# Kernel optimization log

Measured on AMD Instinct MI355X. Metric: run time of the kernel, lower is better.

## Reference

```python
import jax, jax.numpy as jnp
import numpy as np
import math

DIM = 2880
N_HEADS = 64
N_KV = 8
HEAD_DIM = 64
WINDOW = 128          # layer_id = 0 (even) -> sliding window active
BASE = 150000.0
INIT_CTX = 4096
SCALE = 32.0
NTK_ALPHA = 1.0
NTK_BETA = 32.0
EPS = 1e-5
SEQ = 1536
BATCH = 1
SM_SCALE = 1.0 / math.sqrt(HEAD_DIM)


def _rope_tables(seq_len):
    """YaRN (NTK-by-parts) cos/sin tables, half-split convention. [S, D/2]."""
    freq = BASE ** (np.arange(0, HEAD_DIM, 2, dtype=np.float32) / HEAD_DIM)
    concentration = 0.1 * math.log(SCALE) + 1.0
    d_half = HEAD_DIM / 2
    low = d_half * math.log(INIT_CTX / (NTK_BETA * 2 * math.pi)) / math.log(BASE)
    high = d_half * math.log(INIT_CTX / (NTK_ALPHA * 2 * math.pi)) / math.log(BASE)
    interpolation = 1.0 / (SCALE * freq)
    extrapolation = 1.0 / freq
    ramp = (np.arange(d_half, dtype=np.float32) - low) / (high - low)
    mask = 1.0 - np.clip(ramp, 0.0, 1.0)
    inv_freq = interpolation * (1.0 - mask) + extrapolation * mask
    t = np.arange(seq_len, dtype=np.float32)
    freqs = np.outer(t, inv_freq)
    return (jnp.asarray(np.cos(freqs) * concentration),
            jnp.asarray(np.sin(freqs) * concentration))


def _apply_rope(x, cos, sin):
    # x: [B, S, H, D]; cos/sin: [S, D/2]
    c = cos[None, :, None, :]
    s = sin[None, :, None, :]
    x1, x2 = jnp.split(x, 2, axis=-1)
    return jnp.concatenate([x1 * c - x2 * s, x2 * c + x1 * s], axis=-1)


def setup_inputs() -> dict:
    key = jax.random.key(0)
    ks = jax.random.split(key, 5)
    x = jax.random.normal(ks[0], (BATCH, SEQ, DIM), dtype=jnp.float32)
    sinks = jax.random.normal(ks[1], (N_HEADS,), dtype=jnp.float32)
    norm_w = jnp.ones((DIM,), dtype=jnp.float32)
    qkv_dim = HEAD_DIM * (N_HEADS + 2 * N_KV)  # 5120
    qkv_w = jax.random.normal(ks[2], (qkv_dim, DIM), dtype=jnp.float32) / math.sqrt(DIM)
    qkv_b = jnp.zeros((qkv_dim,), dtype=jnp.float32)
    out_w = jax.random.normal(ks[3], (DIM, N_HEADS * HEAD_DIM), dtype=jnp.float32) / math.sqrt(N_HEADS * HEAD_DIM)
    out_b = jnp.zeros((DIM,), dtype=jnp.float32)
    return {"x": x, "sinks": sinks, "norm_w": norm_w, "qkv_w": qkv_w,
            "qkv_b": qkv_b, "out_w": out_w, "out_b": out_b}


def reference(x, sinks, norm_w, qkv_w, qkv_b, out_w, out_b):
    B, S, _ = x.shape
    # RMSNorm
    t = x * jax.lax.rsqrt(jnp.mean(x * x, axis=-1, keepdims=True) + EPS) * norm_w
    # fused QKV projection
    qkv = t @ qkv_w.T + qkv_b
    q_dim = N_HEADS * HEAD_DIM
    kv_dim = N_KV * HEAD_DIM
    q = qkv[..., :q_dim].reshape(B, S, N_HEADS, HEAD_DIM)
    k = qkv[..., q_dim:q_dim + kv_dim].reshape(B, S, N_KV, HEAD_DIM)
    v = qkv[..., q_dim + kv_dim:].reshape(B, S, N_KV, HEAD_DIM)
    # YaRN RoPE
    cos, sin = _rope_tables(S)
    q = _apply_rope(q, cos, sin)
    k = _apply_rope(k, cos, sin)
    # GQA: group query heads per kv head
    G = N_HEADS // N_KV
    qg = q.reshape(B, S, N_KV, G, HEAD_DIM)
    scores = jnp.einsum('bqkgd,bskd->bkgqs', qg, k) * SM_SCALE  # [B,KV,G,Sq,Sk]
    # causal + sliding-window mask
    i = jnp.arange(S)[:, None]
    j = jnp.arange(S)[None, :]
    allowed = j <= i
    if WINDOW > 0:
        allowed = allowed & ((i - j) < WINDOW)
    scores = jnp.where(allowed, scores, -jnp.inf)
    # sink tokens: one extra learned logit per head in the softmax denominator
    sink = sinks.reshape(N_KV, G)[None, :, :, None, None]
    sink = jnp.broadcast_to(sink, (B, N_KV, G, S, 1))
    logits = jnp.concatenate([scores, sink], axis=-1)  # [B,KV,G,Sq,Sk+1]
    p = jax.nn.softmax(logits, axis=-1)[..., :S]        # drop sink column
    attn = jnp.einsum('bkgqs,bskd->bqkgd', p, v).reshape(B, S, N_HEADS * HEAD_DIM)
    return attn @ out_w.T + out_b
```

## Files before the change

### kernel.cpp

```cpp
#include <hip/hip_runtime.h>

typedef unsigned short u16;
typedef unsigned int u32;
typedef __bf16 bf16x8 __attribute__((ext_vector_type(8)));
typedef float f32x4 __attribute__((ext_vector_type(4)));

#define S_LEN 1536
#define DIM 2880
#define NQH 64
#define NKVH 8
#define HD 64
#define QKV_N 5120
#define QDIM 4096
#define KVDIM 512
#define WIN 128
#define SM_SCALE 0.125f

__device__ __forceinline__ u16 f2bf(float f) {
  union { float f; u32 u; } a; a.f = f;
  u32 u = a.u;
  u32 lsb = (u >> 16) & 1;
  u += 0x7fffu + lsb;
  return (u16)(u >> 16);
}
__device__ __forceinline__ u32 pk2bf(float a, float b) {
  return (u32)f2bf(a) | ((u32)f2bf(b) << 16);
}

#define GLOAD16(g, l) __builtin_amdgcn_global_load_lds( \
    (const __attribute__((address_space(1))) u32*)(g), \
    (__attribute__((address_space(3))) u32*)(l), 16, 0, 0)

__global__ void rope_tables(float* __restrict__ cosT, float* __restrict__ sinT) {
  int idx = blockIdx.x * blockDim.x + threadIdx.x;
  if (idx >= S_LEN * 32) return;
  int s = idx >> 5, d = idx & 31;
  const double TWO_PI = 6.283185307179586;
  double freq = pow(150000.0, (double)d / 32.0);
  double conc = 0.1 * log(32.0) + 1.0;
  double lb = log(150000.0);
  double low = 32.0 * log(4096.0 / (32.0 * TWO_PI)) / lb;
  double high = 32.0 * log(4096.0 / (1.0 * TWO_PI)) / lb;
  double interp = 1.0 / (32.0 * freq), extra = 1.0 / freq;
  double ramp = ((double)d - low) / (high - low);
  ramp = ramp < 0.0 ? 0.0 : (ramp > 1.0 ? 1.0 : ramp);
  double maskv = 1.0 - ramp;
  double invf = interp * (1.0 - maskv) + extra * maskv;
  double ang = (double)s * invf;
  cosT[idx] = (float)(cos(ang) * conc);
  sinT[idx] = (float)(sin(ang) * conc);
}

__global__ __launch_bounds__(256) void rmsnorm_bf16(
    const float* __restrict__ x, const float* __restrict__ wgt,
    u16* __restrict__ th) {
  int row = blockIdx.x;
  const float* xr = x + (size_t)row * DIM;
  float ss = 0.f;
  for (int i = threadIdx.x; i < DIM / 4; i += 256) {
    float4 v = *(const float4*)&xr[i * 4];
    ss += v.x * v.x + v.y * v.y + v.z * v.z + v.w * v.w;
  }
  for (int m = 32; m >= 1; m >>= 1) ss += __shfl_xor(ss, m);
  __shared__ float red[4];
  int lane = threadIdx.x & 63, w = threadIdx.x >> 6;
  if (lane == 0) red[w] = ss;
  __syncthreads();
  float tot = red[0] + red[1] + red[2] + red[3];
  float scale = rsqrtf(tot / (float)DIM + 1e-5f);
  for (int i = threadIdx.x; i < DIM / 4; i += 256) {
    float4 v = *(const float4*)&xr[i * 4];
    float4 g = *(const float4*)&wgt[i * 4];
    ushort4 hi;
    hi.x = f2bf(v.x * scale * g.x);
    hi.y = f2bf(v.y * scale * g.y);
    hi.z = f2bf(v.z * scale * g.z);
    hi.w = f2bf(v.w * scale * g.w);
    *(ushort4*)&th[(size_t)row * DIM + i * 4] = hi;
  }
}

__global__ __launch_bounds__(256) void conv2(
    const float* __restrict__ s1, u16* __restrict__ d1, long n1,
    const float* __restrict__ s2, u16* __restrict__ d2, long n2) {
  long idx = (long)blockIdx.x * 256 + threadIdx.x;
  const float* src; u16* dst; long i;
  if (idx < n1) { src = s1; dst = d1; i = idx; }
  else if (idx < n1 + n2) { src = s2; dst = d2; i = idx - n1; }
  else return;
  float4 v = *(const float4*)&src[i * 4];
  ushort4 h;
  h.x = f2bf(v.x); h.y = f2bf(v.y); h.z = f2bf(v.z); h.w = f2bf(v.w);
  *(ushort4*)&dst[i * 4] = h;
}


__global__ __launch_bounds__(256, 4) void gemm_rope(
    const u16* __restrict__ A, const u16* __restrict__ B,
    const float* __restrict__ bias,
    const float* __restrict__ cosT, const float* __restrict__ sinT,
    u16* __restrict__ Qb, u16* __restrict__ Kb, u16* __restrict__ Vt) {
  __shared__ u16 As[3 * 2048];
  __shared__ u16 Bs[3 * 4096];
  const int K = DIM;
  const int t = threadIdx.x;
  const int lane = t & 63, w = t >> 6;

  const int nby = gridDim.y;
  const int nwg = gridDim.x * nby;
  int orig = blockIdx.x * nby + blockIdx.y;
  {
    int q = nwg >> 3, r = nwg & 7;
    int xcd = orig & 7, i = orig >> 3;
    orig = (xcd < r ? xcd * (q + 1) : r * (q + 1) + (xcd - r) * q) + i;
  }
  const int m0 = (orig % nby) * 64, n0 = (orig / nby) * 128;

  const int wr = (w >> 1) * 32, wc = (w & 1) * 64;
  const int lr = lane & 15, lk8 = (lane >> 4) * 8;
  const int lcol = lk8 ^ (((lr >> 1) & 3) << 3);
  const int g4 = (lane >> 4) * 4;
  f32x4 acc[2][4] = {};

  const size_t ga  = (size_t)(m0 + (t >> 2)) * K + (((t & 3) ^ ((t >> 3) & 3)) * 8);
  const size_t gb0 = (size_t)(n0 + (t >> 2)) * K + (((t & 3) ^ ((t >> 3) & 3)) * 8);
  const size_t gb1 = (size_t)(n0 + 64 + (t >> 2)) * K + (((t & 3) ^ ((t >> 3) & 3)) * 8);

  auto STAGE = [&](int buf, int k0) {
    GLOAD16(A + ga + k0,  &As[buf * 2048 + t * 8]);
    GLOAD16(B + gb0 + k0, &Bs[buf * 4096 + t * 8]);
    GLOAD16(B + gb1 + k0, &Bs[buf * 4096 + (t + 256) * 8]);
  };

  const int nk = K / 32;
  STAGE(0, 0); STAGE(1, 32);

  for (int tt = 0; tt < nk; ++tt) {
    const int cur = tt % 3;
    if (tt + 1 < nk) {
      asm volatile("s_waitcnt vmcnt(6)" ::: "memory");
    } else {
      asm volatile("s_waitcnt vmcnt(0)" ::: "memory");
    }
    __builtin_amdgcn_s_barrier();
    __builtin_amdgcn_sched_barrier(0);
    if (tt + 2 < nk) STAGE((tt + 2) % 3, (tt + 2) * 32);
    const u16* as_ = &As[cur * 2048];
    const u16* bs_ = &Bs[cur * 4096];
    bf16x8 af[2], bf_[4];
#pragma unroll
    for (int i = 0; i < 2; ++i) af[i] = *(const bf16x8*)&as_[(wr + i * 16 + lr) * 32 + lcol];
#pragma unroll
    for (int j = 0; j < 4; ++j) bf_[j] = *(const bf16x8*)&bs_[(wc + j * 16 + lr) * 32 + lcol];
    __builtin_amdgcn_s_setprio(1);
#pragma unroll
    for (int i = 0; i < 2; ++i)
#pragma unroll
      for (int j = 0; j < 4; ++j)
        acc[i][j] = __builtin_amdgcn_mfma_f32_16x16x32_bf16(af[i], bf_[j], acc[i][j], 0, 0, 0);
    __builtin_amdgcn_s_setprio(0);
  }

  if (n0 < 4608) {
    const bool isQ = (n0 < 4096);
    const float sc = isQ ? SM_SCALE : 1.0f;
#pragma unroll
    for (int i = 0; i < 2; ++i) {
      const int row = m0 + wr + i * 16 + g4;
#pragma unroll
      for (int j = 0; j < 2; ++j) {
        const int col = n0 + wc + j * 16 + lr;
        const int d = j * 16 + lr;
        const float b1 = bias[col], b2 = bias[col + 32];
#pragma unroll
        for (int r = 0; r < 4; ++r) {
          const float c = cosT[(row + r) * 32 + d];
          const float s = sinT[(row + r) * 32 + d];
          const float x1 = acc[i][j][r] + b1;
          const float x2 = acc[i][j + 2][r] + b2;
          const float o1 = (x1 * c - x2 * s) * sc;
          const float o2 = (x2 * c + x1 * s) * sc;
          if (isQ) {
            Qb[(size_t)(row + r) * QDIM + col] = f2bf(o1);
            Qb[(size_t)(row + r) * QDIM + col + 32] = f2bf(o2);
          } else {
            Kb[(size_t)(row + r) * KVDIM + (col - 4096)] = f2bf(o1);
            Kb[(size_t)(row + r) * KVDIM + (col - 4096) + 32] = f2bf(o2);
          }
        }
      }
    }
  } else {
#pragma unroll
    for (int i = 0; i < 2; ++i) {
      const int rowb = m0 + wr + i * 16 + g4;
#pragma unroll
      for (int j = 0; j < 4; ++j) {
        const int col = n0 + wc + j * 16 + lr;
        const float bb = bias[col];
        ushort4 pk;
        pk.x = f2bf(acc[i][j][0] + bb);
        pk.y = f2bf(acc[i][j][1] + bb);
        pk.z = f2bf(acc[i][j][2] + bb);
        pk.w = f2bf(acc[i][j][3] + bb);
        *(ushort4*)&Vt[(size_t)(col - 4608) * S_LEN + rowb] = pk;
      }
    }
  }
}

__global__ __launch_bounds__(256, 4) void gemm_bt(
    const u16* __restrict__ A, const u16* __restrict__ B,
    const float* __restrict__ bias, float* __restrict__ C,
    int M, int N, int K) {
  __shared__ u16 As[3 * 2048];
  __shared__ u16 Bs[3 * 4096];
  const int t = threadIdx.x;
  const int lane = t & 63, w = t >> 6;

  const int nby = gridDim.y;
  const int nwg = gridDim.x * nby;
  int orig = blockIdx.x * nby + blockIdx.y;
  {
    int q = nwg >> 3, r = nwg & 7;
    int xcd = orig & 7, i = orig >> 3;
    orig = (xcd < r ? xcd * (q + 1) : r * (q + 1) + (xcd - r) * q) + i;
  }
  const int m0 = (orig % nby) * 64, n0 = (orig / nby) * 128;

  const int wr = (w >> 1) * 32, wc = (w & 1) * 64;
  const int lr = lane & 15, lk8 = (lane >> 4) * 8;
  const int lcol = lk8 ^ (((lr >> 1) & 3) << 3);
  const int g4 = (lane >> 4) * 4;
  f32x4 acc[2][4] = {};

  int rB0 = n0 + (t >> 2); if (rB0 > N - 1) rB0 = N - 1;
  int rB1 = n0 + 64 + (t >> 2); if (rB1 > N - 1) rB1 = N - 1;
  const size_t ga  = (size_t)(m0 + (t >> 2)) * K + (((t & 3) ^ ((t >> 3) & 3)) * 8);
  const size_t gb0 = (size_t)rB0 * K + (((t & 3) ^ ((t >> 3) & 3)) * 8);
  const size_t gb1 = (size_t)rB1 * K + (((t & 3) ^ ((t >> 3) & 3)) * 8);

  auto STAGE = [&](int buf, int k0) {
    GLOAD16(A + ga + k0,  &As[buf * 2048 + t * 8]);
    GLOAD16(B + gb0 + k0, &Bs[buf * 4096 + t * 8]);
    GLOAD16(B + gb1 + k0, &Bs[buf * 4096 + (t + 256) * 8]);
  };

  const int nk = K / 32;
  STAGE(0, 0); STAGE(1, 32);

  for (int tt = 0; tt < nk; ++tt) {
    const int cur = tt % 3;
    if (tt + 1 < nk) {
      asm volatile("s_waitcnt vmcnt(6)" ::: "memory");
    } else {
      asm volatile("s_waitcnt vmcnt(0)" ::: "memory");
    }
    __builtin_amdgcn_s_barrier();
    __builtin_amdgcn_sched_barrier(0);
    if (tt + 2 < nk) STAGE((tt + 2) % 3, (tt + 2) * 32);
    const u16* as_ = &As[cur * 2048];
    const u16* bs_ = &Bs[cur * 4096];
    bf16x8 af[2], bf_[4];
#pragma unroll
    for (int i = 0; i < 2; ++i) af[i] = *(const bf16x8*)&as_[(wr + i * 16 + lr) * 32 + lcol];
#pragma unroll
    for (int j = 0; j < 4; ++j) bf_[j] = *(const bf16x8*)&bs_[(wc + j * 16 + lr) * 32 + lcol];
    __builtin_amdgcn_s_setprio(1);
#pragma unroll
    for (int i = 0; i < 2; ++i)
#pragma unroll
      for (int j = 0; j < 4; ++j)
        acc[i][j] = __builtin_amdgcn_mfma_f32_16x16x32_bf16(af[i], bf_[j], acc[i][j], 0, 0, 0);
    __builtin_amdgcn_s_setprio(0);
  }

#pragma unroll
  for (int i = 0; i < 2; ++i) {
    const int row = m0 + wr + i * 16 + g4;
#pragma unroll
    for (int j = 0; j < 4; ++j) {
      const int col = n0 + wc + j * 16 + lr;
      if (col < N) {
        const float bb = bias[col];
#pragma unroll
        for (int r = 0; r < 4; ++r)
          C[(size_t)(row + r) * N + col] = acc[i][j][r] + bb;
      }
    }
  }
}

__global__ __launch_bounds__(256) void attn2(
    const u16* __restrict__ Q, const u16* __restrict__ Kb, const u16* __restrict__ Vt,
    const float* __restrict__ sinks, u16* __restrict__ O) {
  const int h = blockIdx.x;
  const int kh = h >> 3;
  const int wid = threadIdx.x >> 6;
  const int lane = threadIdx.x & 63;
  const int q0 = blockIdx.y * 128 + wid * 32;
  const int lr = lane & 15;
  const int g = lane >> 4;

  bf16x8 bq[2][2];
#pragma unroll
  for (int qf = 0; qf < 2; ++qf)
#pragma unroll
    for (int kc = 0; kc < 2; ++kc)
      bq[qf][kc] = *(const bf16x8*)&Q[(size_t)(q0 + qf * 16 + lr) * QDIM + h * HD + kc * 32 + g * 8];

  f32x4 o[2][4] = {};
  float m_s[2] = {-1e30f, -1e30f};
  float l_s[2] = {0.f, 0.f};

  int js = q0 - 128; if (js < 0) js = 0;

  for (int j0 = js; j0 <= q0; j0 += 32) {
    bf16x8 ak[2][2];
#pragma unroll
    for (int jf = 0; jf < 2; ++jf)
#pragma unroll
      for (int kc = 0; kc < 2; ++kc)
        ak[jf][kc] = *(const bf16x8*)&Kb[(size_t)(j0 + jf * 16 + lr) * KVDIM + kh * HD + kc * 32 + g * 8];

    f32x4 st[2][2] = {};
#pragma unroll
    for (int jf = 0; jf < 2; ++jf)
#pragma unroll
      for (int qf = 0; qf < 2; ++qf) {
        st[jf][qf] = __builtin_amdgcn_mfma_f32_16x16x32_bf16(ak[jf][0], bq[qf][0], st[jf][qf], 0, 0, 0);
        st[jf][qf] = __builtin_amdgcn_mfma_f32_16x16x32_bf16(ak[jf][1], bq[qf][1], st[jf][qf], 0, 0, 0);
      }

    float pv[2][2][4];
    float tmax[2] = {-1e30f, -1e30f};
#pragma unroll
    for (int jf = 0; jf < 2; ++jf)
#pragma unroll
      for (int qf = 0; qf < 2; ++qf)
#pragma unroll
        for (int r = 0; r < 4; ++r) {
          int jv = j0 + jf * 16 + 4 * g + r;
          int qq = q0 + qf * 16 + lr;
          float sc = st[jf][qf][r];
          bool ok = (jv <= qq) && (qq - jv < WIN);
          sc = ok ? sc : -1e30f;
          pv[jf][qf][r] = sc;
          tmax[qf] = fmaxf(tmax[qf], sc);
        }
#pragma unroll
    for (int qf = 0; qf < 2; ++qf) {
      float tm = tmax[qf];
      tm = fmaxf(tm, __shfl_xor(tm, 16));
      tm = fmaxf(tm, __shfl_xor(tm, 32));
      const float mo = m_s[qf];
      const float mn = fmaxf(mo, tm);
      const float esc = __expf(mo - mn);
      float ps = 0.f;
#pragma unroll
      for (int jf = 0; jf < 2; ++jf)
#pragma unroll
        for (int r = 0; r < 4; ++r) {
          float sv = pv[jf][qf][r];
          float e = __expf(sv - mn);
          e = (sv <= -1e29f) ? 0.f : e;
          pv[jf][qf][r] = e;
          ps += e;
        }
      ps += __shfl_xor(ps, 16);
      ps += __shfl_xor(ps, 32);
      l_s[qf] = l_s[qf] * esc + ps;
      m_s[qf] = mn;
#pragma unroll
      for (int df = 0; df < 4; ++df) o[qf][df] *= esc;
    }

    bf16x8 pb[2];
    const int srcA = lr + ((g & 1) ? 32 : 0);
    const int srcB = srcA + 16;
    const bool hi_half = (g >= 2);
#pragma unroll
    for (int qf = 0; qf < 2; ++qf) {
      u32 w0a = pk2bf(pv[0][qf][0], pv[0][qf][1]);
      u32 w1a = pk2bf(pv[0][qf][2], pv[0][qf][3]);
      u32 w0b = pk2bf(pv[1][qf][0], pv[1][qf][1]);
      u32 w1b = pk2bf(pv[1][qf][2], pv[1][qf][3]);
      u32 a0 = (u32)__shfl((int)w0a, srcA, 64);
      u32 a1 = (u32)__shfl((int)w1a, srcA, 64);
      u32 a2 = (u32)__shfl((int)w0a, srcB, 64);
      u32 a3 = (u32)__shfl((int)w1a, srcB, 64);
      u32 b0 = (u32)__shfl((int)w0b, srcA, 64);
      u32 b1 = (u32)__shfl((int)w1b, srcA, 64);
      u32 b2 = (u32)__shfl((int)w0b, srcB, 64);
      u32 b3 = (u32)__shfl((int)w1b, srcB, 64);
      union { u32 d[4]; bf16x8 v; } u_;
      u_.d[0] = hi_half ? b0 : a0;
      u_.d[1] = hi_half ? b1 : a1;
      u_.d[2] = hi_half ? b2 : a2;
      u_.d[3] = hi_half ? b3 : a3;
      pb[qf] = u_.v;
    }

    bf16x8 av[4];
#pragma unroll
    for (int df = 0; df < 4; ++df)
      av[df] = *(const bf16x8*)&Vt[((size_t)kh * HD + df * 16 + lr) * S_LEN + j0 + g * 8];

#pragma unroll
    for (int qf = 0; qf < 2; ++qf)
#pragma unroll
      for (int df = 0; df < 4; ++df)
        o[qf][df] = __builtin_amdgcn_mfma_f32_16x16x32_bf16(av[df], pb[qf], o[qf][df], 0, 0, 0);
  }

  const float snk = sinks[h];
#pragma unroll
  for (int qf = 0; qf < 2; ++qf) {
    const float mo = m_s[qf];
    const float Mx = fmaxf(mo, snk);
    const float den = l_s[qf] * __expf(mo - Mx) + __expf(snk - Mx);
    const float osc = __expf(mo - Mx) / den;
    const int row = q0 + qf * 16 + lr;
#pragma unroll
    for (int df = 0; df < 4; ++df) {
      ushort4 pk;
      pk.x = f2bf(o[qf][df][0] * osc);
      pk.y = f2bf(o[qf][df][1] * osc);
      pk.z = f2bf(o[qf][df][2] * osc);
      pk.w = f2bf(o[qf][df][3] * osc);
      *(ushort4*)&O[(size_t)row * QDIM + h * HD + df * 16 + 4 * g] = pk;
    }
  }
}

extern "C" void kernel_launch(void* const* d_in, const int* in_sizes, int n_in,
                              void* d_out, int out_size, void* d_ws, size_t ws_size,
                              hipStream_t stream) {
  const float* x      = (const float*)d_in[0];
  const float* sinks  = (const float*)d_in[1];
  const float* norm_w = (const float*)d_in[2];
  const float* qkv_w  = (const float*)d_in[3];
  const float* qkv_b  = (const float*)d_in[4];
  const float* out_w  = (const float*)d_in[5];
  const float* out_b  = (const float*)d_in[6];
  float* out = (float*)d_out;

  char* ws = (char*)d_ws;
  size_t off = 0;
  auto take = [&](size_t bytes) -> void* {
    void* r = ws + off;
    off += (bytes + 255) & ~(size_t)255;
    return r;
  };
  float* cosT = (float*)take((size_t)S_LEN * 32 * 4);
  float* sinT = (float*)take((size_t)S_LEN * 32 * 4);
  u16* th  = (u16*)take((size_t)S_LEN * DIM * 2);
  u16* wh  = (u16*)take((size_t)QKV_N * DIM * 2);
  u16* ow  = (u16*)take((size_t)DIM * QDIM * 2);
  u16* Qb  = (u16*)take((size_t)S_LEN * QDIM * 2);
  u16* Kb  = (u16*)take((size_t)S_LEN * KVDIM * 2);
  u16* Vt  = (u16*)take((size_t)S_LEN * KVDIM * 2);
  u16* Ab  = (u16*)take((size_t)S_LEN * QDIM * 2);

  const long n1 = (long)QKV_N * DIM / 4;
  const long n2 = (long)DIM * QDIM / 4;

  rope_tables<<<(S_LEN * 32 + 255) / 256, 256, 0, stream>>>(cosT, sinT);
  rmsnorm_bf16<<<S_LEN, 256, 0, stream>>>(x, norm_w, th);
  conv2<<<(int)((n1 + n2 + 255) / 256), 256, 0, stream>>>(qkv_w, wh, n1, out_w, ow, n2);
  gemm_rope<<<dim3(QKV_N / 128, S_LEN / 64), 256, 0, stream>>>(
      th, wh, qkv_b, cosT, sinT, Qb, Kb, Vt);
  attn2<<<dim3(NQH, S_LEN / 128), 256, 0, stream>>>(Qb, Kb, Vt, sinks, Ab);
  gemm_bt<<<dim3((DIM + 127) / 128, S_LEN / 64), 256, 0, stream>>>(
      Ab, ow, out_b, out, S_LEN, DIM, QDIM);
}
```

Before: 216.6 us.

## Enlarge GEMM tiles to 128x128 and issue prefetch before the wait

Both bf16 GEMMs (QKV+RoPE and output projection) now compute 128x128 output tiles per block, with each wave holding a 64x64 accumulator, instead of 64x128. This halves the A/B tile reloads from global memory and raises MFMA work per LDS read. The next-stage global load is now issued before the vmcnt wait, with an extra end-of-iteration barrier protecting buffer reuse. The trade-offs are higher register and LDS use (occupancy hint lowered to 3) and a grid of fewer blocks, which may leave CUs idle or poorly balanced.

```diff
diff --git a/kernel.cpp b/kernel.cpp
--- a/kernel.cpp
+++ b/kernel.cpp
@@ -95,12 +95,12 @@
 }
 
 
-__global__ __launch_bounds__(256, 4) void gemm_rope(
+__global__ __launch_bounds__(256, 3) void gemm_rope(
     const u16* __restrict__ A, const u16* __restrict__ B,
     const float* __restrict__ bias,
     const float* __restrict__ cosT, const float* __restrict__ sinT,
     u16* __restrict__ Qb, u16* __restrict__ Kb, u16* __restrict__ Vt) {
-  __shared__ u16 As[3 * 2048];
+  __shared__ u16 As[3 * 4096];
   __shared__ u16 Bs[3 * 4096];
   const int K = DIM;
   const int t = threadIdx.x;
@@ -114,20 +114,23 @@
     int xcd = orig & 7, i = orig >> 3;
     orig = (xcd < r ? xcd * (q + 1) : r * (q + 1) + (xcd - r) * q) + i;
   }
-  const int m0 = (orig % nby) * 64, n0 = (orig / nby) * 128;
-
-  const int wr = (w >> 1) * 32, wc = (w & 1) * 64;
+  const int m0 = (orig % nby) * 128, n0 = (orig / nby) * 128;
+
+  const int wr = (w >> 1) * 64, wc = (w & 1) * 64;
   const int lr = lane & 15, lk8 = (lane >> 4) * 8;
   const int lcol = lk8 ^ (((lr >> 1) & 3) << 3);
   const int g4 = (lane >> 4) * 4;
-  f32x4 acc[2][4] = {};
-
-  const size_t ga  = (size_t)(m0 + (t >> 2)) * K + (((t & 3) ^ ((t >> 3) & 3)) * 8);
-  const size_t gb0 = (size_t)(n0 + (t >> 2)) * K + (((t & 3) ^ ((t >> 3) & 3)) * 8);
-  const size_t gb1 = (size_t)(n0 + 64 + (t >> 2)) * K + (((t & 3) ^ ((t >> 3) & 3)) * 8);
+  f32x4 acc[4][4] = {};
+
+  const int ks = ((t & 3) ^ ((t >> 3) & 3)) * 8;
+  const size_t ga0 = (size_t)(m0 + (t >> 2)) * K + ks;
+  const size_t ga1 = (size_t)(m0 + 64 + (t >> 2)) * K + ks;
+  const size_t gb0 = (size_t)(n0 + (t >> 2)) * K + ks;
+  const size_t gb1 = (size_t)(n0 + 64 + (t >> 2)) * K + ks;
 
   auto STAGE = [&](int buf, int k0) {
-    GLOAD16(A + ga + k0,  &As[buf * 2048 + t * 8]);
+    GLOAD16(A + ga0 + k0, &As[buf * 4096 + t * 8]);
+    GLOAD16(A + ga1 + k0, &As[buf * 4096 + (t + 256) * 8]);
     GLOAD16(B + gb0 + k0, &Bs[buf * 4096 + t * 8]);
     GLOAD16(B + gb1 + k0, &Bs[buf * 4096 + (t + 256) * 8]);
   };
@@ -137,35 +140,39 @@
 
   for (int tt = 0; tt < nk; ++tt) {
     const int cur = tt % 3;
-    if (tt + 1 < nk) {
-      asm volatile("s_waitcnt vmcnt(6)" ::: "memory");
+    if (tt + 2 < nk) {
+      STAGE((tt + 2) % 3, (tt + 2) * 32);
+      asm volatile("s_waitcnt vmcnt(8)" ::: "memory");
+    } else if (tt + 1 < nk) {
+      asm volatile("s_waitcnt vmcnt(4)" ::: "memory");
     } else {
       asm volatile("s_waitcnt vmcnt(0)" ::: "memory");
     }
     __builtin_amdgcn_s_barrier();
     __builtin_amdgcn_sched_barrier(0);
-    if (tt + 2 < nk) STAGE((tt + 2) % 3, (tt + 2) * 32);
-    const u16* as_ = &As[cur * 2048];
+    const u16* as_ = &As[cur * 4096];
     const u16* bs_ = &Bs[cur * 4096];
-    bf16x8 af[2], bf_[4];
-#pragma unroll
-    for (int i = 0; i < 2; ++i) af[i] = *(const bf16x8*)&as_[(wr + i * 16 + lr) * 32 + lcol];
+    bf16x8 af[4], bf_[4];
+#pragma unroll
+    for (int i = 0; i < 4; ++i) af[i] = *(const bf16x8*)&as_[(wr + i * 16 + lr) * 32 + lcol];
 #pragma unroll
     for (int j = 0; j < 4; ++j) bf_[j] = *(const bf16x8*)&bs_[(wc + j * 16 + lr) * 32 + lcol];
     __builtin_amdgcn_s_setprio(1);
 #pragma unroll
-    for (int i = 0; i < 2; ++i)
+    for (int i = 0; i < 4; ++i)
 #pragma unroll
       for (int j = 0; j < 4; ++j)
         acc[i][j] = __builtin_amdgcn_mfma_f32_16x16x32_bf16(af[i], bf_[j], acc[i][j], 0, 0, 0);
     __builtin_amdgcn_s_setprio(0);
+    __builtin_amdgcn_sched_barrier(0);
+    __builtin_amdgcn_s_barrier();
   }
 
   if (n0 < 4608) {
     const bool isQ = (n0 < 4096);
     const float sc = isQ ? SM_SCALE : 1.0f;
 #pragma unroll
-    for (int i = 0; i < 2; ++i) {
+    for (int i = 0; i < 4; ++i) {
       const int row = m0 + wr + i * 16 + g4;
 #pragma unroll
       for (int j = 0; j < 2; ++j) {
@@ -192,7 +199,7 @@
     }
   } else {
 #pragma unroll
-    for (int i = 0; i < 2; ++i) {
+    for (int i = 0; i < 4; ++i) {
       const int rowb = m0 + wr + i * 16 + g4;
 #pragma unroll
       for (int j = 0; j < 4; ++j) {
@@ -209,11 +216,11 @@
   }
 }
 
-__global__ __launch_bounds__(256, 4) void gemm_bt(
+__global__ __launch_bounds__(256, 3) void gemm_bt(
     const u16* __restrict__ A, const u16* __restrict__ B,
     const float* __restrict__ bias, float* __restrict__ C,
     int M, int N, int K) {
-  __shared__ u16 As[3 * 2048];
+  __shared__ u16 As[3 * 4096];
   __shared__ u16 Bs[3 * 4096];
   const int t = threadIdx.x;
   const int lane = t & 63, w = t >> 6;
@@ -226,22 +233,25 @@
     int xcd = orig & 7, i = orig >> 3;
     orig = (xcd < r ? xcd * (q + 1) : r * (q + 1) + (xcd - r) * q) + i;
   }
-  const int m0 = (orig % nby) * 64, n0 = (orig / nby) * 128;
-
-  const int wr = (w >> 1) * 32, wc = (w & 1) * 64;
+  const int m0 = (orig % nby) * 128, n0 = (orig / nby) * 128;
+
+  const int wr = (w >> 1) * 64, wc = (w & 1) * 64;
   const int lr = lane & 15, lk8 = (lane >> 4) * 8;
   const int lcol = lk8 ^ (((lr >> 1) & 3) << 3);
   const int g4 = (lane >> 4) * 4;
-  f32x4 acc[2][4] = {};
-
+  f32x4 acc[4][4] = {};
+
+  const int ks = ((t & 3) ^ ((t >> 3) & 3)) * 8;
   int rB0 = n0 + (t >> 2); if (rB0 > N - 1) rB0 = N - 1;
   int rB1 = n0 + 64 + (t >> 2); if (rB1 > N - 1) rB1 = N - 1;
-  const size_t ga  = (size_t)(m0 + (t >> 2)) * K + (((t & 3) ^ ((t >> 3) & 3)) * 8);
-  const size_t gb0 = (size_t)rB0 * K + (((t & 3) ^ ((t >> 3) & 3)) * 8);
-  const size_t gb1 = (size_t)rB1 * K + (((t & 3) ^ ((t >> 3) & 3)) * 8);
+  const size_t ga0 = (size_t)(m0 + (t >> 2)) * K + ks;
+  const size_t ga1 = (size_t)(m0 + 64 + (t >> 2)) * K + ks;
+  const size_t gb0 = (size_t)rB0 * K + ks;
+  const size_t gb1 = (size_t)rB1 * K + ks;
 
   auto STAGE = [&](int buf, int k0) {
-    GLOAD16(A + ga + k0,  &As[buf * 2048 + t * 8]);
+    GLOAD16(A + ga0 + k0, &As[buf * 4096 + t * 8]);
+    GLOAD16(A + ga1 + k0, &As[buf * 4096 + (t + 256) * 8]);
     GLOAD16(B + gb0 + k0, &Bs[buf * 4096 + t * 8]);
     GLOAD16(B + gb1 + k0, &Bs[buf * 4096 + (t + 256) * 8]);
   };
@@ -251,32 +261,36 @@
 
   for (int tt = 0; tt < nk; ++tt) {
     const int cur = tt % 3;
-    if (tt + 1 < nk) {
-      asm volatile("s_waitcnt vmcnt(6)" ::: "memory");
+    if (tt + 2 < nk) {
+      STAGE((tt + 2) % 3, (tt + 2) * 32);
+      asm volatile("s_waitcnt vmcnt(8)" ::: "memory");
+    } else if (tt + 1 < nk) {
+      asm volatile("s_waitcnt vmcnt(4)" ::: "memory");
     } else {
       asm volatile("s_waitcnt vmcnt(0)" ::: "memory");
     }
     __builtin_amdgcn_s_barrier();
     __builtin_amdgcn_sched_barrier(0);
-    if (tt + 2 < nk) STAGE((tt + 2) % 3, (tt + 2) * 32);
-    const u16* as_ = &As[cur * 2048];
+    const u16* as_ = &As[cur * 4096];
     const u16* bs_ = &Bs[cur * 4096];
-    bf16x8 af[2], bf_[4];
-#pragma unroll
-    for (int i = 0; i < 2; ++i) af[i] = *(const bf16x8*)&as_[(wr + i * 16 + lr) * 32 + lcol];
+    bf16x8 af[4], bf_[4];
+#pragma unroll
+    for (int i = 0; i < 4; ++i) af[i] = *(const bf16x8*)&as_[(wr + i * 16 + lr) * 32 + lcol];
 #pragma unroll
     for (int j = 0; j < 4; ++j) bf_[j] = *(const bf16x8*)&bs_[(wc + j * 16 + lr) * 32 + lcol];
     __builtin_amdgcn_s_setprio(1);
 #pragma unroll
-    for (int i = 0; i < 2; ++i)
+    for (int i = 0; i < 4; ++i)
 #pragma unroll
       for (int j = 0; j < 4; ++j)
         acc[i][j] = __builtin_amdgcn_mfma_f32_16x16x32_bf16(af[i], bf_[j], acc[i][j], 0, 0, 0);
     __builtin_amdgcn_s_setprio(0);
-  }
-
-#pragma unroll
-  for (int i = 0; i < 2; ++i) {
+    __builtin_amdgcn_sched_barrier(0);
+    __builtin_amdgcn_s_barrier();
+  }
+
+#pragma unroll
+  for (int i = 0; i < 4; ++i) {
     const int row = m0 + wr + i * 16 + g4;
 #pragma unroll
     for (int j = 0; j < 4; ++j) {
@@ -468,9 +482,9 @@
   rope_tables<<<(S_LEN * 32 + 255) / 256, 256, 0, stream>>>(cosT, sinT);
   rmsnorm_bf16<<<S_LEN, 256, 0, stream>>>(x, norm_w, th);
   conv2<<<(int)((n1 + n2 + 255) / 256), 256, 0, stream>>>(qkv_w, wh, n1, out_w, ow, n2);
-  gemm_rope<<<dim3(QKV_N / 128, S_LEN / 64), 256, 0, stream>>>(
+  gemm_rope<<<dim3(QKV_N / 128, S_LEN / 128), 256, 0, stream>>>(
       th, wh, qkv_b, cosT, sinT, Qb, Kb, Vt);
   attn2<<<dim3(NQH, S_LEN / 128), 256, 0, stream>>>(Qb, Kb, Vt, sinks, Ab);
-  gemm_bt<<<dim3((DIM + 127) / 128, S_LEN / 64), 256, 0, stream>>>(
+  gemm_bt<<<dim3((DIM + 127) / 128, (S_LEN + 127) / 128), 256, 0, stream>>>(
       Ab, ow, out_b, out, S_LEN, DIM, QDIM);
 }
```

New measurement: 214.8 us. Within noise of the previous version (-0.8%).
